# Performance work log

Measured on AMD Instinct MI355X. Metric: run time of the kernel, lower is better.

The kernel has to match this reference:

```python
import jax, jax.numpy as jnp
import numpy as np

BS, IN_SIZE, OUT_SIZE, FEATS = 32, 1024, 1024, 2048


def setup_inputs() -> dict:
    key = jax.random.key(0)
    kx, kw = jax.random.split(key)
    x = jax.random.normal(kx, (BS, IN_SIZE, FEATS), dtype=jnp.float32)
    # Per-sample weight matrices (the stacked nn.Parameters, kernel-size-1 conv
    # weights of shape [out_size, in_size, 1] -> squeezed to [out_size, in_size]).
    weights = jax.random.normal(kw, (BS, OUT_SIZE, IN_SIZE), dtype=jnp.float32)
    return {"x": x, "weights": weights}


def reference(x, weights):
    # F.conv2d(x.view(1, bs*in_size, feats), W.view(bs*out_size, in_size, 1), groups=bs)
    # with kernel size 1 is exactly a per-sample matmul:
    # out[b, o, f] = sum_i weights[b, o, i] * x[b, i, f]
    return jnp.einsum('boi,bif->bof', weights, x)
```

## Files before the change

### kernel.cpp

```cpp
#include <hip/hip_runtime.h>
#include <hip/hip_bf16.h>
#include <string.h>


typedef float  f32x2 __attribute__((ext_vector_type(2)));
typedef float  f32x4 __attribute__((ext_vector_type(4)));
typedef short  bf16x8 __attribute__((ext_vector_type(8)));
typedef unsigned int u32;

#define BATCH 32
#define MDIM 1024
#define KDIM 1024
#define NDIM 2048
#define BM 256
#define BN 256
#define BK 32
#define NT (KDIM / BK)
#define LSTR 36

__device__ __forceinline__ u32 cvt2(float a, float b) {
    float2 t; t.x = a; t.y = b;
    __hip_bfloat162 h = __float22bfloat162_rn(t);
    u32 r; memcpy(&r, &h, 4);
    return r;
}

__device__ __forceinline__ void lds_barrier() {
    asm volatile("s_waitcnt lgkmcnt(0)" ::: "memory");
    __builtin_amdgcn_s_barrier();
    asm volatile("" ::: "memory");
}

__global__ __launch_bounds__(512, 2) void bgemm_bf16_kernel(
    const float* __restrict__ x, const float* __restrict__ w,
    float* __restrict__ out)
{
    __shared__ unsigned short Ab[2][BM * LSTR];
    __shared__ unsigned short Bb[2][BN * LSTR];

    const int bid  = blockIdx.x;
    const int lbid = (bid & 7) * 128 + (bid >> 3);
    const int bx = lbid & 7;
    const int by = (lbid >> 3) & 3;
    const int bz = lbid >> 5;

    const int tid = threadIdx.x;
    const int m0  = by * BM;
    const int n0  = bx * BN;

    const int lane = tid & 63;
    const int wid  = tid >> 6;
    const int wm   = (wid >> 2) * 128;
    const int wn   = (wid & 3)  * 64;
    const int l15  = lane & 15;
    const int kg8  = (lane >> 4) * 8;

    const float* Ag = w + (size_t)bz * MDIM * KDIM + (size_t)m0 * KDIM;
    const float* Bg = x + (size_t)bz * KDIM * NDIM + n0;
    float*       Cg = out + (size_t)bz * MDIM * NDIM + (size_t)m0 * NDIM + n0;

    const int a_k4 = tid & 7;
    const int a_m0 = tid >> 3;
    int a_idx[4];
    #pragma unroll
    for (int i = 0; i < 4; ++i)
        a_idx[i] = (a_m0 + 64 * i) * LSTR + 4 * a_k4;
    const int bn0  = 2 * (tid & 127);
    const int b_k0 = 8 * (tid >> 7);
    int b_idx[2];
    #pragma unroll
    for (int c = 0; c < 2; ++c)
        b_idx[c] = (bn0 + c) * LSTR + b_k0;
    int rd_a[8], rd_b[4];
    #pragma unroll
    for (int mi = 0; mi < 8; ++mi)
        rd_a[mi] = (wm + mi * 16 + l15) * LSTR + kg8;
    #pragma unroll
    for (int ni = 0; ni < 4; ++ni)
        rd_b[ni] = (wn + ni * 16 + l15) * LSTR + kg8;

    const float* Ap = Ag + (size_t)a_m0 * KDIM + 4 * a_k4;
    const float* Bp = Bg + (size_t)b_k0 * NDIM + bn0;

    f32x4 acc[8][4];
    #pragma unroll
    for (int i = 0; i < 8; ++i)
        #pragma unroll
        for (int j = 0; j < 4; ++j)
            acc[i][j] = f32x4{0.f, 0.f, 0.f, 0.f};

    f32x4 aav[4];
    f32x2 bbv[8];

    auto load_regs = [&](int kt) {
        #pragma unroll
        for (int i = 0; i < 4; ++i)
            aav[i] = *reinterpret_cast<const f32x4*>(Ap + (size_t)(64 * i) * KDIM + kt);
        #pragma unroll
        for (int j = 0; j < 8; ++j)
            bbv[j] = *reinterpret_cast<const f32x2*>(Bp + (size_t)(kt + j) * NDIM);
    };
    auto stage = [&](int s) {
        #pragma unroll
        for (int i = 0; i < 4; ++i) {
            uint2 v = make_uint2(cvt2(aav[i][0], aav[i][1]),
                                 cvt2(aav[i][2], aav[i][3]));
            *reinterpret_cast<uint2*>(&Ab[s][a_idx[i]]) = v;
        }
        #pragma unroll
        for (int c = 0; c < 2; ++c) {
            uint4 v = make_uint4(cvt2(bbv[0][c], bbv[1][c]),
                                 cvt2(bbv[2][c], bbv[3][c]),
                                 cvt2(bbv[4][c], bbv[5][c]),
                                 cvt2(bbv[6][c], bbv[7][c]));
            *reinterpret_cast<uint4*>(&Bb[s][b_idx[c]]) = v;
        }
    };

    load_regs(0);
    stage(0);
    load_regs(BK);
    lds_barrier();

    for (int t = 0; t < NT - 1; ++t) {
        const int cur = t & 1;
        bf16x8 bfr[4], af1[4];

        #pragma unroll
        for (int ni = 0; ni < 4; ++ni)
            bfr[ni] = *reinterpret_cast<const bf16x8*>(&Bb[cur][rd_b[ni]]);
        #pragma unroll
        for (int mi = 0; mi < 4; ++mi)
            af1[mi] = *reinterpret_cast<const bf16x8*>(&Ab[cur][rd_a[mi]]);

        stage(cur ^ 1);

        __builtin_amdgcn_s_setprio(1);
        #pragma unroll
        for (int mi = 0; mi < 4; ++mi)
            #pragma unroll
            for (int ni = 0; ni < 4; ++ni)
                acc[mi][ni] = __builtin_amdgcn_mfma_f32_16x16x32_bf16(
                    af1[mi], bfr[ni], acc[mi][ni], 0, 0, 0);
        __builtin_amdgcn_s_setprio(0);

        bf16x8 af2[4];
        #pragma unroll
        for (int mi = 0; mi < 4; ++mi)
            af2[mi] = *reinterpret_cast<const bf16x8*>(&Ab[cur][rd_a[mi + 4]]);
        int kt2 = (t + 2) * BK;
        if (kt2 > KDIM - BK) kt2 = KDIM - BK;
        load_regs(kt2);

        __builtin_amdgcn_s_setprio(1);
        #pragma unroll
        for (int mi = 0; mi < 4; ++mi)
            #pragma unroll
            for (int ni = 0; ni < 4; ++ni)
                acc[mi + 4][ni] = __builtin_amdgcn_mfma_f32_16x16x32_bf16(
                    af2[mi], bfr[ni], acc[mi + 4][ni], 0, 0, 0);
        __builtin_amdgcn_s_setprio(0);

        lds_barrier();
    }

    {
        const int cur = (NT - 1) & 1;
        bf16x8 bfr[4];
        #pragma unroll
        for (int ni = 0; ni < 4; ++ni)
            bfr[ni] = *reinterpret_cast<const bf16x8*>(&Bb[cur][rd_b[ni]]);
        #pragma unroll
        for (int mi = 0; mi < 8; ++mi) {
            bf16x8 af = *reinterpret_cast<const bf16x8*>(&Ab[cur][rd_a[mi]]);
            #pragma unroll
            for (int ni = 0; ni < 4; ++ni)
                acc[mi][ni] = __builtin_amdgcn_mfma_f32_16x16x32_bf16(
                    af, bfr[ni], acc[mi][ni], 0, 0, 0);
        }
    }

    const int rbase = (lane >> 4) * 4;
    #pragma unroll
    for (int mi = 0; mi < 8; ++mi) {
        #pragma unroll
        for (int ni = 0; ni < 4; ++ni) {
            int n  = wn + ni * 16 + l15;
            int mb = wm + mi * 16 + rbase;
            #pragma unroll
            for (int r = 0; r < 4; ++r)
                Cg[(size_t)(mb + r) * NDIM + n] = acc[mi][ni][r];
        }
    }
}

extern "C" void kernel_launch(void* const* d_in, const int* in_sizes, int n_in,
                              void* d_out, int out_size, void* d_ws, size_t ws_size,
                              hipStream_t stream) {
    const float* x = (const float*)d_in[0];
    const float* w = (const float*)d_in[1];
    float* out = (float*)d_out;
    const int nblocks = (NDIM / BN) * (MDIM / BM) * BATCH;
    bgemm_bf16_kernel<<<dim3(nblocks), dim3(512), 0, stream>>>(x, w, out);
}
```

Baseline: 250.8 us.

## Double the K tile to 64 and split staging into two overlapped halves

Raises the K tile from 32 to 64, which halves the number of main-loop iterations and block barriers. Each half of the next tile's global loads and bf16 LDS stores is interleaved between MFMA groups so the copy overlaps the math. The A-tile thread mapping and the LDS stride change to fit the wider tile. The LDS footprint roughly doubles, so the two blocks per CU requested by the launch bounds may no longer fit, and register pressure rises.

```diff
diff --git a/kernel.cpp b/kernel.cpp
--- a/kernel.cpp
+++ b/kernel.cpp
@@ -14,9 +14,9 @@
 #define NDIM 2048
 #define BM 256
 #define BN 256
-#define BK 32
+#define BK 64
 #define NT (KDIM / BK)
-#define LSTR 36
+#define LSTR 68
 
 __device__ __forceinline__ u32 cvt2(float a, float b) {
     float2 t; t.x = a; t.y = b;
@@ -59,12 +59,12 @@
     const float* Bg = x + (size_t)bz * KDIM * NDIM + n0;
     float*       Cg = out + (size_t)bz * MDIM * NDIM + (size_t)m0 * NDIM + n0;
 
-    const int a_k4 = tid & 7;
-    const int a_m0 = tid >> 3;
-    int a_idx[4];
-    #pragma unroll
-    for (int i = 0; i < 4; ++i)
-        a_idx[i] = (a_m0 + 64 * i) * LSTR + 4 * a_k4;
+    const int a_k4 = tid & 15;
+    const int a_m0 = tid >> 4;
+    int a_idx[8];
+    #pragma unroll
+    for (int i = 0; i < 8; ++i)
+        a_idx[i] = (a_m0 + 32 * i) * LSTR + 4 * a_k4;
     const int bn0  = 2 * (tid & 127);
     const int b_k0 = 8 * (tid >> 7);
     int b_idx[2];
@@ -92,20 +92,22 @@
     f32x4 aav[4];
     f32x2 bbv[8];
 
-    auto load_regs = [&](int kt) {
+    auto load_regs = [&](int kt, int h) {
         #pragma unroll
         for (int i = 0; i < 4; ++i)
-            aav[i] = *reinterpret_cast<const f32x4*>(Ap + (size_t)(64 * i) * KDIM + kt);
+            aav[i] = *reinterpret_cast<const f32x4*>(
+                Ap + (size_t)(32 * (i + 4 * h)) * KDIM + kt);
         #pragma unroll
         for (int j = 0; j < 8; ++j)
-            bbv[j] = *reinterpret_cast<const f32x2*>(Bp + (size_t)(kt + j) * NDIM);
+            bbv[j] = *reinterpret_cast<const f32x2*>(
+                Bp + (size_t)(kt + 32 * h + j) * NDIM);
     };
-    auto stage = [&](int s) {
+    auto stage = [&](int s, int h) {
         #pragma unroll
         for (int i = 0; i < 4; ++i) {
             uint2 v = make_uint2(cvt2(aav[i][0], aav[i][1]),
                                  cvt2(aav[i][2], aav[i][3]));
-            *reinterpret_cast<uint2*>(&Ab[s][a_idx[i]]) = v;
+            *reinterpret_cast<uint2*>(&Ab[s][a_idx[i + 4 * h]]) = v;
         }
         #pragma unroll
         for (int c = 0; c < 2; ++c) {
@@ -113,27 +115,31 @@
                                  cvt2(bbv[2][c], bbv[3][c]),
                                  cvt2(bbv[4][c], bbv[5][c]),
                                  cvt2(bbv[6][c], bbv[7][c]));
-            *reinterpret_cast<uint4*>(&Bb[s][b_idx[c]]) = v;
+            *reinterpret_cast<uint4*>(&Bb[s][b_idx[c] + 32 * h]) = v;
         }
     };
 
-    load_regs(0);
-    stage(0);
-    load_regs(BK);
+    load_regs(0, 0);
+    stage(0, 0);
+    load_regs(0, 1);
+    stage(0, 1);
+    load_regs(BK, 0);
     lds_barrier();
 
     for (int t = 0; t < NT - 1; ++t) {
         const int cur = t & 1;
-        bf16x8 bfr[4], af1[4];
+        const int ktn = (t + 1) * BK;
+        bf16x8 bfr[4], af[4];
 
         #pragma unroll
         for (int ni = 0; ni < 4; ++ni)
             bfr[ni] = *reinterpret_cast<const bf16x8*>(&Bb[cur][rd_b[ni]]);
         #pragma unroll
         for (int mi = 0; mi < 4; ++mi)
-            af1[mi] = *reinterpret_cast<const bf16x8*>(&Ab[cur][rd_a[mi]]);
-
-        stage(cur ^ 1);
+            af[mi] = *reinterpret_cast<const bf16x8*>(&Ab[cur][rd_a[mi]]);
+
+        stage(cur ^ 1, 0);
+        load_regs(ktn, 1);
 
         __builtin_amdgcn_s_setprio(1);
         #pragma unroll
@@ -141,16 +147,46 @@
             #pragma unroll
             for (int ni = 0; ni < 4; ++ni)
                 acc[mi][ni] = __builtin_amdgcn_mfma_f32_16x16x32_bf16(
-                    af1[mi], bfr[ni], acc[mi][ni], 0, 0, 0);
-        __builtin_amdgcn_s_setprio(0);
-
-        bf16x8 af2[4];
-        #pragma unroll
-        for (int mi = 0; mi < 4; ++mi)
-            af2[mi] = *reinterpret_cast<const bf16x8*>(&Ab[cur][rd_a[mi + 4]]);
+                    af[mi], bfr[ni], acc[mi][ni], 0, 0, 0);
+        __builtin_amdgcn_s_setprio(0);
+
+        #pragma unroll
+        for (int mi = 0; mi < 4; ++mi)
+            af[mi] = *reinterpret_cast<const bf16x8*>(&Ab[cur][rd_a[mi + 4]]);
+
+        __builtin_amdgcn_s_setprio(1);
+        #pragma unroll
+        for (int mi = 0; mi < 4; ++mi)
+            #pragma unroll
+            for (int ni = 0; ni < 4; ++ni)
+                acc[mi + 4][ni] = __builtin_amdgcn_mfma_f32_16x16x32_bf16(
+                    af[mi], bfr[ni], acc[mi + 4][ni], 0, 0, 0);
+        __builtin_amdgcn_s_setprio(0);
+
+        #pragma unroll
+        for (int ni = 0; ni < 4; ++ni)
+            bfr[ni] = *reinterpret_cast<const bf16x8*>(&Bb[cur][rd_b[ni] + 32]);
+        #pragma unroll
+        for (int mi = 0; mi < 4; ++mi)
+            af[mi] = *reinterpret_cast<const bf16x8*>(&Ab[cur][rd_a[mi] + 32]);
+
+        stage(cur ^ 1, 1);
         int kt2 = (t + 2) * BK;
         if (kt2 > KDIM - BK) kt2 = KDIM - BK;
-        load_regs(kt2);
+        load_regs(kt2, 0);
+
+        __builtin_amdgcn_s_setprio(1);
+        #pragma unroll
+        for (int mi = 0; mi < 4; ++mi)
+            #pragma unroll
+            for (int ni = 0; ni < 4; ++ni)
+                acc[mi][ni] = __builtin_amdgcn_mfma_f32_16x16x32_bf16(
+                    af[mi], bfr[ni], acc[mi][ni], 0, 0, 0);
+        __builtin_amdgcn_s_setprio(0);
+
+        #pragma unroll
+        for (int mi = 0; mi < 4; ++mi)
+            af[mi] = *reinterpret_cast<const bf16x8*>(&Ab[cur][rd_a[mi + 4] + 32]);
 
         __builtin_amdgcn_s_setprio(1);
         #pragma unroll
@@ -158,7 +194,7 @@
             #pragma unroll
             for (int ni = 0; ni < 4; ++ni)
                 acc[mi + 4][ni] = __builtin_amdgcn_mfma_f32_16x16x32_bf16(
-                    af2[mi], bfr[ni], acc[mi + 4][ni], 0, 0, 0);
+                    af[mi], bfr[ni], acc[mi + 4][ni], 0, 0, 0);
         __builtin_amdgcn_s_setprio(0);
 
         lds_barrier();
@@ -166,17 +202,22 @@
 
     {
         const int cur = (NT - 1) & 1;
-        bf16x8 bfr[4];
-        #pragma unroll
-        for (int ni = 0; ni < 4; ++ni)
-            bfr[ni] = *reinterpret_cast<const bf16x8*>(&Bb[cur][rd_b[ni]]);
-        #pragma unroll
-        for (int mi = 0; mi < 8; ++mi) {
-            bf16x8 af = *reinterpret_cast<const bf16x8*>(&Ab[cur][rd_a[mi]]);
-            #pragma unroll
-            for (int ni = 0; ni < 4; ++ni)
-                acc[mi][ni] = __builtin_amdgcn_mfma_f32_16x16x32_bf16(
-                    af, bfr[ni], acc[mi][ni], 0, 0, 0);
+        #pragma unroll
+        for (int kk = 0; kk < 2; ++kk) {
+            bf16x8 bfr[4];
+            #pragma unroll
+            for (int ni = 0; ni < 4; ++ni)
+                bfr[ni] = *reinterpret_cast<const bf16x8*>(
+                    &Bb[cur][rd_b[ni] + 32 * kk]);
+            #pragma unroll
+            for (int mi = 0; mi < 8; ++mi) {
+                bf16x8 af = *reinterpret_cast<const bf16x8*>(
+                    &Ab[cur][rd_a[mi] + 32 * kk]);
+                #pragma unroll
+                for (int ni = 0; ni < 4; ++ni)
+                    acc[mi][ni] = __builtin_amdgcn_mfma_f32_16x16x32_bf16(
+                        af, bfr[ni], acc[mi][ni], 0, 0, 0);
+            }
         }
     }
 
```

Measured after the change: 231.9 us. 1.08x faster.
